# Kernel tuning notes

Measured on AMD Instinct MI355X. Metric: run time of the kernel, lower is better.

Reference implementation:

```python
import jax, jax.numpy as jnp
import numpy as np

N_NODES = 50000
N_EDGES = 640000
IN_CH = 128
OUT_CH = 128


def setup_inputs() -> dict:
    key = jax.random.key(0)
    k1, k2, k3, k4 = jax.random.split(key, 4)
    x = jax.random.normal(k1, (N_NODES, IN_CH), dtype=jnp.float32)
    edge_index = jax.random.randint(k2, (2, N_EDGES), 0, N_NODES, dtype=jnp.int32)
    # nn.Linear params: W [out, in], b [out]
    bound = 1.0 / np.sqrt(IN_CH)
    W = jax.random.uniform(k3, (OUT_CH, IN_CH), minval=-bound, maxval=bound, dtype=jnp.float32)
    b = jax.random.uniform(k4, (OUT_CH,), minval=-bound, maxval=bound, dtype=jnp.float32)
    return {"x": x, "edge_index": edge_index, "W": W, "b": b}


def reference(x, edge_index, W, b):
    row, col = edge_index[0], edge_index[1]
    num_nodes = x.shape[0]
    # degree of each destination node (clamped to >= 1)
    deg = jax.ops.segment_sum(jnp.ones(row.shape[0], dtype=x.dtype), row,
                              num_segments=num_nodes)
    deg = jnp.maximum(deg, 1.0)
    # gather neighbor features and scatter-add into destinations
    agg = jax.ops.segment_sum(x[col], row, num_segments=num_nodes)
    agg = agg / deg[:, None]
    # residual + linear
    return (x + agg) @ W.T + b
```

## Files before the change

### kernel.cpp

```cpp
#include <hip/hip_runtime.h>

#define N_NODES 50000
#define N_EDGES 640000
#define CH 128
#define NBINS 1563
#define NTILES 1563
#define BINB 256
#define EPB 2500
#define CAPR 48

typedef __bf16 bf16_t;
typedef bf16_t bf16x8 __attribute__((ext_vector_type(8)));
typedef float f32x4 __attribute__((ext_vector_type(4)));

__device__ __forceinline__ ushort f2bf(float f) {
  union { float f; unsigned u; } v; v.f = f;
  unsigned r = v.u + 0x7FFFu + ((v.u >> 16) & 1u);
  return (ushort)(r >> 16);
}
__device__ __forceinline__ float bflo(unsigned u) {
  union { unsigned u; float f; } v; v.u = u << 16; return v.f;
}
__device__ __forceinline__ float bfhi(unsigned u) {
  union { unsigned u; float f; } v; v.u = u & 0xFFFF0000u; return v.f;
}
__device__ __forceinline__ unsigned pack2(float lo, float hi) {
  return (unsigned)f2bf(lo) | ((unsigned)f2bf(hi) << 16);
}
__device__ __forceinline__ void addrow(float* acc, uint4 v) {
  acc[0] += bflo(v.x); acc[1] += bfhi(v.x);
  acc[2] += bflo(v.y); acc[3] += bfhi(v.y);
  acc[4] += bflo(v.z); acc[5] += bfhi(v.z);
  acc[6] += bflo(v.w); acc[7] += bfhi(v.w);
}


__global__ __launch_bounds__(256) void bink(const int* __restrict__ row,
                                            const int* __restrict__ col,
                                            unsigned* __restrict__ binRec,
                                            ushort* __restrict__ obot) {
  __shared__ int cnt[NBINS];
  __shared__ int parts[256];
  __shared__ __align__(16) unsigned recbuf[EPB];
  int bid = blockIdx.x;
  int tid = threadIdx.x;
  for (int i = tid; i < NBINS; i += 256) cnt[i] = 0;
  __syncthreads();
  int base = bid * EPB;
  int4 r4s[3], c4s[3];
  bool val[3];
#pragma unroll
  for (int b = 0; b < 3; ++b) {
    int idx4 = b * 1024 + tid * 4;
    val[b] = idx4 < EPB;
    if (val[b]) {
      r4s[b] = *(const int4*)(row + base + idx4);
      c4s[b] = *(const int4*)(col + base + idx4);
    }
  }
  unsigned pkv[12];
  unsigned colp[6];
#pragma unroll
  for (int b = 0; b < 3; ++b) {
    if (val[b]) {
      int rr[4] = {r4s[b].x, r4s[b].y, r4s[b].z, r4s[b].w};
      int cc[4] = {c4s[b].x, c4s[b].y, c4s[b].z, c4s[b].w};
#pragma unroll
      for (int j = 0; j < 4; ++j) {
        int bi = rr[j] >> 5;
        int rk = atomicAdd(&cnt[bi], 1);
        pkv[b * 4 + j] = ((unsigned)bi << 13) |
                         ((unsigned)(rr[j] & 31) << 8) | (unsigned)rk;
      }
      colp[b * 2]     = ((unsigned)cc[0] & 0xFFFFu) | ((unsigned)cc[1] << 16);
      colp[b * 2 + 1] = ((unsigned)cc[2] & 0xFFFFu) | ((unsigned)cc[3] << 16);
    } else {
#pragma unroll
      for (int j = 0; j < 4; ++j) pkv[b * 4 + j] = 0xFFFFFFFFu;
      colp[b * 2] = 0; colp[b * 2 + 1] = 0;
    }
  }
  __syncthreads();
  int c7[7];
  int s = 0;
#pragma unroll
  for (int k = 0; k < 7; ++k) {
    int i = tid * 7 + k;
    int c = (i < NBINS) ? cnt[i] : 0;
    c7[k] = c; s += c;
  }
  parts[tid] = s;
  __syncthreads();
  for (int off = 1; off < 256; off <<= 1) {
    int v = (tid >= off) ? parts[tid - off] : 0;
    __syncthreads();
    parts[tid] += v;
    __syncthreads();
  }
  int run = (tid > 0) ? parts[tid - 1] : 0;
#pragma unroll
  for (int k = 0; k < 7; ++k) {
    int i = tid * 7 + k;
    if (i < NBINS) {
      obot[i * BINB + bid] = (ushort)run;
      cnt[i] = run;
      run += c7[k];
    }
  }
  if (tid == 0) obot[NBINS * BINB + bid] = (ushort)EPB;
  __syncthreads();
#pragma unroll
  for (int k = 0; k < 12; ++k) {
    unsigned p = pkv[k];
    if (p != 0xFFFFFFFFu) {
      int bi = (int)(p >> 13);
      int lr5 = (int)((p >> 8) & 31u);
      int rk = (int)(p & 255u);
      unsigned cw = (colp[k >> 1] >> ((k & 1) * 16)) & 0xFFFFu;
      recbuf[cnt[bi] + rk] = ((unsigned)lr5 << 16) | cw;
    }
  }
  __syncthreads();
  uint4* gb4 = (uint4*)(binRec + base);
  const uint4* rb4 = (const uint4*)recbuf;
  for (int j = tid; j < EPB / 4; j += 256) gb4[j] = rb4[j];
}

__global__ __launch_bounds__(256) void conv(const float4* __restrict__ x4,
                                            uint4* __restrict__ xb4,
                                            const float4* __restrict__ W4,
                                            uint4* __restrict__ Wb4) {
  int bid = blockIdx.x;
  int tid = threadIdx.x;
  if (bid < 3125) {
    int i = bid * 256 + tid;
    float4 a = x4[i * 2], b = x4[i * 2 + 1];
    uint4 o;
    o.x = pack2(a.x, a.y); o.y = pack2(a.z, a.w);
    o.z = pack2(b.x, b.y); o.w = pack2(b.z, b.w);
    xb4[i] = o;
  } else {
    for (int i = tid; i < 2048; i += 256) {
      float4 c = W4[i * 2], d = W4[i * 2 + 1];
      uint4 w;
      w.x = pack2(c.x, c.y); w.y = pack2(c.z, c.w);
      w.z = pack2(d.x, d.y); w.w = pack2(d.z, d.w);
      Wb4[i] = w;
    }
  }
}

__global__ __launch_bounds__(512) void fused(const uint4* __restrict__ xb4,
                                             const unsigned* __restrict__ binRec,
                                             const ushort* __restrict__ obot,
                                             const uint4* __restrict__ Wb4,
                                             const float4* __restrict__ bias4,
                                             float4* __restrict__ out4) {
  __shared__ ushort hT[32 * CH];
  __shared__ __align__(16) ushort colL[32 * CAPR];
  __shared__ int rowcnt[32];
  int tid = threadIdx.x;
  int g = blockIdx.x;
  int m0 = g * 32;

  if (tid < 32) rowcnt[tid] = 0;
  __syncthreads();
  {
    int i = tid >> 1, sub = tid & 1;
    int o0 = obot[g * BINB + i];
    int o1 = obot[(g + 1) * BINB + i];
    const unsigned* rbase = binRec + i * EPB;
    for (int p = o0 + sub; p < o1; p += 2) {
      unsigned rec = rbase[p];
      int lr = (int)(rec >> 16);
      int pp = atomicAdd(&rowcnt[lr], 1);
      if (pp < CAPR) colL[lr * CAPR + pp] = (ushort)(rec & 0xFFFFu);
    }
  }
  __syncthreads();

  int wv = tid >> 6;
  int lane = tid & 63;
  int q = lane & 15;
  int grp = lane >> 4;
  int r = wv * 4 + grp;
  int node = m0 + r;
  int deg = rowcnt[r];
  int degc = deg < CAPR ? deg : CAPR;
  const ushort* arow = colL + r * CAPR;
  int nc = node < N_NODES ? node : 0;
  uint4 xi = xb4[nc * 16 + q];
  float acc[8] = {0.f, 0.f, 0.f, 0.f, 0.f, 0.f, 0.f, 0.f};
  int e = 0;
  for (; e + 7 < degc; e += 8) {
    uint4 ids = *(const uint4*)(arow + e);
    int n0 = ids.x & 0xFFFF, n1 = ids.x >> 16;
    int n2 = ids.y & 0xFFFF, n3 = ids.y >> 16;
    int n4 = ids.z & 0xFFFF, n5 = ids.z >> 16;
    int n6 = ids.w & 0xFFFF, n7 = ids.w >> 16;
    uint4 v0 = xb4[n0 * 16 + q];
    uint4 v1 = xb4[n1 * 16 + q];
    uint4 v2 = xb4[n2 * 16 + q];
    uint4 v3 = xb4[n3 * 16 + q];
    uint4 v4 = xb4[n4 * 16 + q];
    uint4 v5 = xb4[n5 * 16 + q];
    uint4 v6 = xb4[n6 * 16 + q];
    uint4 v7 = xb4[n7 * 16 + q];
    addrow(acc, v0); addrow(acc, v1); addrow(acc, v2); addrow(acc, v3);
    addrow(acc, v4); addrow(acc, v5); addrow(acc, v6); addrow(acc, v7);
  }
  if (e + 3 < degc) {
    uint2 ids = *(const uint2*)(arow + e);
    int n0 = ids.x & 0xFFFF, n1 = ids.x >> 16;
    int n2 = ids.y & 0xFFFF, n3 = ids.y >> 16;
    uint4 v0 = xb4[n0 * 16 + q];
    uint4 v1 = xb4[n1 * 16 + q];
    uint4 v2 = xb4[n2 * 16 + q];
    uint4 v3 = xb4[n3 * 16 + q];
    addrow(acc, v0); addrow(acc, v1); addrow(acc, v2); addrow(acc, v3);
    e += 4;
  }
  for (; e < degc; ++e) {
    uint4 v = xb4[(int)arow[e] * 16 + q];
    addrow(acc, v);
  }
  uint4 o = make_uint4(0, 0, 0, 0);
  if (node < N_NODES) {
    float s = 1.0f / fmaxf((float)deg, 1.0f);
    o.x = pack2(bflo(xi.x) + acc[0] * s, bfhi(xi.x) + acc[1] * s);
    o.y = pack2(bflo(xi.y) + acc[2] * s, bfhi(xi.y) + acc[3] * s);
    o.z = pack2(bflo(xi.z) + acc[4] * s, bfhi(xi.z) + acc[5] * s);
    o.w = pack2(bflo(xi.w) + acc[6] * s, bfhi(xi.w) + acc[7] * s);
  }
  *(uint4*)&hT[r * CH + ((q ^ (r & 15)) << 3)] = o;
  __syncthreads();

  int qq = grp;
  int mt = wv & 1;
  int nbase = (wv >> 1) * 2;
  const ushort* hbase = &hT[(mt * 16 + q) * CH];
  bf16x8 hb0 = *(const bf16x8*)(hbase + (((qq + 0) ^ q) << 3));
  bf16x8 hb1 = *(const bf16x8*)(hbase + (((qq + 4) ^ q) << 3));
  bf16x8 hb2 = *(const bf16x8*)(hbase + (((qq + 8) ^ q) << 3));
  bf16x8 hb3 = *(const bf16x8*)(hbase + (((qq + 12) ^ q) << 3));
  int m = m0 + mt * 16 + q;
#pragma unroll
  for (int i = 0; i < 2; ++i) {
    int nt = nbase + i;
    const uint4* wr = Wb4 + (nt * 16 + q) * 16 + qq;
    bf16x8 w0 = __builtin_bit_cast(bf16x8, wr[0]);
    bf16x8 w1 = __builtin_bit_cast(bf16x8, wr[4]);
    bf16x8 w2 = __builtin_bit_cast(bf16x8, wr[8]);
    bf16x8 w3 = __builtin_bit_cast(bf16x8, wr[12]);
    f32x4 acc2 = {0.f, 0.f, 0.f, 0.f};
    acc2 = __builtin_amdgcn_mfma_f32_16x16x32_bf16(w0, hb0, acc2, 0, 0, 0);
    acc2 = __builtin_amdgcn_mfma_f32_16x16x32_bf16(w1, hb1, acc2, 0, 0, 0);
    acc2 = __builtin_amdgcn_mfma_f32_16x16x32_bf16(w2, hb2, acc2, 0, 0, 0);
    acc2 = __builtin_amdgcn_mfma_f32_16x16x32_bf16(w3, hb3, acc2, 0, 0, 0);
    if (m < N_NODES) {
      float4 bv = bias4[nt * 4 + qq];
      f32x4 ov;
      ov.x = acc2[0] + bv.x;
      ov.y = acc2[1] + bv.y;
      ov.z = acc2[2] + bv.z;
      ov.w = acc2[3] + bv.w;
      __builtin_nontemporal_store(ov, (f32x4*)(out4 + (size_t)m * 32 + nt * 4 + qq));
    }
  }
}

extern "C" void kernel_launch(void* const* d_in, const int* in_sizes, int n_in,
                              void* d_out, int out_size, void* d_ws, size_t ws_size,
                              hipStream_t stream) {
  const float* x  = (const float*)d_in[0];
  const int*   ei = (const int*)d_in[1];
  const float* W  = (const float*)d_in[2];
  const float* bb = (const float*)d_in[3];

  char* ws = (char*)d_ws;
  unsigned* binRec = (unsigned*)ws;
  ushort*   obot   = (ushort*)(ws + 2560000);
  uint4*    Wb4    = (uint4*)(ws + 3360768);
  uint4*    xb4    = (uint4*)(ws + 3393536);

  bink<<<BINB, 256, 0, stream>>>(ei, ei + N_EDGES, binRec, obot);
  conv<<<3126, 256, 0, stream>>>((const float4*)x, xb4, (const float4*)W, Wb4);
  fused<<<NTILES, 512, 0, stream>>>(xb4, binRec, obot, Wb4,
                                    (const float4*)bb, (float4*)d_out);
}
```

Before: 133.1 us.

## Merge binning and bf16 conversion kernels, pad neighbor lists with zero row

The edge-binning kernel and the x/W bf16 conversion kernel become one launch, with branches on block index, so the two independent prep stages overlap and one launch is saved. Loads of x now use nontemporal hints. In the fused kernel each row's neighbor list is padded up to a multiple of 8 with a sentinel index that points at an extra zeroed row of xb4. This removes the 4-wide and scalar tail loops at the cost of extra gathers from that zero row. The zero row is written past the end of xb4, so the workspace must have room for it.

```diff
diff --git a/kernel.cpp b/kernel.cpp
--- a/kernel.cpp
+++ b/kernel.cpp
@@ -8,6 +8,7 @@
 #define BINB 256
 #define EPB 2500
 #define CAPR 48
+#define ZID N_NODES
 
 typedef __bf16 bf16_t;
 typedef bf16_t bf16x8 __attribute__((ext_vector_type(8)));
@@ -35,109 +36,107 @@
 }
 
 
-__global__ __launch_bounds__(256) void bink(const int* __restrict__ row,
+__global__ __launch_bounds__(256) void prep(const int* __restrict__ row,
                                             const int* __restrict__ col,
                                             unsigned* __restrict__ binRec,
-                                            ushort* __restrict__ obot) {
+                                            ushort* __restrict__ obot,
+                                            const f32x4* __restrict__ x4,
+                                            uint4* __restrict__ xb4,
+                                            const float4* __restrict__ W4,
+                                            uint4* __restrict__ Wb4) {
   __shared__ int cnt[NBINS];
   __shared__ int parts[256];
   __shared__ __align__(16) unsigned recbuf[EPB];
   int bid = blockIdx.x;
   int tid = threadIdx.x;
-  for (int i = tid; i < NBINS; i += 256) cnt[i] = 0;
-  __syncthreads();
-  int base = bid * EPB;
-  int4 r4s[3], c4s[3];
-  bool val[3];
-#pragma unroll
-  for (int b = 0; b < 3; ++b) {
-    int idx4 = b * 1024 + tid * 4;
-    val[b] = idx4 < EPB;
-    if (val[b]) {
-      r4s[b] = *(const int4*)(row + base + idx4);
-      c4s[b] = *(const int4*)(col + base + idx4);
-    }
-  }
-  unsigned pkv[12];
-  unsigned colp[6];
-#pragma unroll
-  for (int b = 0; b < 3; ++b) {
-    if (val[b]) {
-      int rr[4] = {r4s[b].x, r4s[b].y, r4s[b].z, r4s[b].w};
-      int cc[4] = {c4s[b].x, c4s[b].y, c4s[b].z, c4s[b].w};
-#pragma unroll
-      for (int j = 0; j < 4; ++j) {
-        int bi = rr[j] >> 5;
-        int rk = atomicAdd(&cnt[bi], 1);
-        pkv[b * 4 + j] = ((unsigned)bi << 13) |
-                         ((unsigned)(rr[j] & 31) << 8) | (unsigned)rk;
-      }
-      colp[b * 2]     = ((unsigned)cc[0] & 0xFFFFu) | ((unsigned)cc[1] << 16);
-      colp[b * 2 + 1] = ((unsigned)cc[2] & 0xFFFFu) | ((unsigned)cc[3] << 16);
-    } else {
-#pragma unroll
-      for (int j = 0; j < 4; ++j) pkv[b * 4 + j] = 0xFFFFFFFFu;
-      colp[b * 2] = 0; colp[b * 2 + 1] = 0;
-    }
-  }
-  __syncthreads();
-  int c7[7];
-  int s = 0;
-#pragma unroll
-  for (int k = 0; k < 7; ++k) {
-    int i = tid * 7 + k;
-    int c = (i < NBINS) ? cnt[i] : 0;
-    c7[k] = c; s += c;
-  }
-  parts[tid] = s;
-  __syncthreads();
-  for (int off = 1; off < 256; off <<= 1) {
-    int v = (tid >= off) ? parts[tid - off] : 0;
-    __syncthreads();
-    parts[tid] += v;
-    __syncthreads();
-  }
-  int run = (tid > 0) ? parts[tid - 1] : 0;
-#pragma unroll
-  for (int k = 0; k < 7; ++k) {
-    int i = tid * 7 + k;
-    if (i < NBINS) {
-      obot[i * BINB + bid] = (ushort)run;
-      cnt[i] = run;
-      run += c7[k];
-    }
-  }
-  if (tid == 0) obot[NBINS * BINB + bid] = (ushort)EPB;
-  __syncthreads();
-#pragma unroll
-  for (int k = 0; k < 12; ++k) {
-    unsigned p = pkv[k];
-    if (p != 0xFFFFFFFFu) {
-      int bi = (int)(p >> 13);
-      int lr5 = (int)((p >> 8) & 31u);
-      int rk = (int)(p & 255u);
-      unsigned cw = (colp[k >> 1] >> ((k & 1) * 16)) & 0xFFFFu;
-      recbuf[cnt[bi] + rk] = ((unsigned)lr5 << 16) | cw;
-    }
-  }
-  __syncthreads();
-  uint4* gb4 = (uint4*)(binRec + base);
-  const uint4* rb4 = (const uint4*)recbuf;
-  for (int j = tid; j < EPB / 4; j += 256) gb4[j] = rb4[j];
-}
-
-__global__ __launch_bounds__(256) void conv(const float4* __restrict__ x4,
-                                            uint4* __restrict__ xb4,
-                                            const float4* __restrict__ W4,
-                                            uint4* __restrict__ Wb4) {
-  int bid = blockIdx.x;
-  int tid = threadIdx.x;
-  if (bid < 3125) {
-    int i = bid * 256 + tid;
-    float4 a = x4[i * 2], b = x4[i * 2 + 1];
+  if (bid < BINB) {
+    for (int i = tid; i < NBINS; i += 256) cnt[i] = 0;
+    __syncthreads();
+    int base = bid * EPB;
+    int4 r4s[3], c4s[3];
+    bool val[3];
+#pragma unroll
+    for (int b = 0; b < 3; ++b) {
+      int idx4 = b * 1024 + tid * 4;
+      val[b] = idx4 < EPB;
+      if (val[b]) {
+        r4s[b] = *(const int4*)(row + base + idx4);
+        c4s[b] = *(const int4*)(col + base + idx4);
+      }
+    }
+    unsigned pkv[12];
+    unsigned colp[6];
+#pragma unroll
+    for (int b = 0; b < 3; ++b) {
+      if (val[b]) {
+        int rr[4] = {r4s[b].x, r4s[b].y, r4s[b].z, r4s[b].w};
+        int cc[4] = {c4s[b].x, c4s[b].y, c4s[b].z, c4s[b].w};
+#pragma unroll
+        for (int j = 0; j < 4; ++j) {
+          int bi = rr[j] >> 5;
+          int rk = atomicAdd(&cnt[bi], 1);
+          pkv[b * 4 + j] = ((unsigned)bi << 13) |
+                           ((unsigned)(rr[j] & 31) << 8) | (unsigned)rk;
+        }
+        colp[b * 2]     = ((unsigned)cc[0] & 0xFFFFu) | ((unsigned)cc[1] << 16);
+        colp[b * 2 + 1] = ((unsigned)cc[2] & 0xFFFFu) | ((unsigned)cc[3] << 16);
+      } else {
+#pragma unroll
+        for (int j = 0; j < 4; ++j) pkv[b * 4 + j] = 0xFFFFFFFFu;
+        colp[b * 2] = 0; colp[b * 2 + 1] = 0;
+      }
+    }
+    __syncthreads();
+    int c7[7];
+    int s = 0;
+#pragma unroll
+    for (int k = 0; k < 7; ++k) {
+      int i = tid * 7 + k;
+      int c = (i < NBINS) ? cnt[i] : 0;
+      c7[k] = c; s += c;
+    }
+    parts[tid] = s;
+    __syncthreads();
+    for (int off = 1; off < 256; off <<= 1) {
+      int v = (tid >= off) ? parts[tid - off] : 0;
+      __syncthreads();
+      parts[tid] += v;
+      __syncthreads();
+    }
+    int run = (tid > 0) ? parts[tid - 1] : 0;
+#pragma unroll
+    for (int k = 0; k < 7; ++k) {
+      int i = tid * 7 + k;
+      if (i < NBINS) {
+        obot[i * BINB + bid] = (ushort)run;
+        cnt[i] = run;
+        run += c7[k];
+      }
+    }
+    if (tid == 0) obot[NBINS * BINB + bid] = (ushort)EPB;
+    __syncthreads();
+#pragma unroll
+    for (int k = 0; k < 12; ++k) {
+      unsigned p = pkv[k];
+      if (p != 0xFFFFFFFFu) {
+        int bi = (int)(p >> 13);
+        int lr5 = (int)((p >> 8) & 31u);
+        int rk = (int)(p & 255u);
+        unsigned cw = (colp[k >> 1] >> ((k & 1) * 16)) & 0xFFFFu;
+        recbuf[cnt[bi] + rk] = ((unsigned)lr5 << 16) | cw;
+      }
+    }
+    __syncthreads();
+    uint4* gb4 = (uint4*)(binRec + base);
+    const uint4* rb4 = (const uint4*)recbuf;
+    for (int j = tid; j < EPB / 4; j += 256) gb4[j] = rb4[j];
+  } else if (bid < BINB + 3125) {
+    int i = (bid - BINB) * 256 + tid;
+    f32x4 a = __builtin_nontemporal_load(x4 + i * 2);
+    f32x4 b = __builtin_nontemporal_load(x4 + i * 2 + 1);
     uint4 o;
-    o.x = pack2(a.x, a.y); o.y = pack2(a.z, a.w);
-    o.z = pack2(b.x, b.y); o.w = pack2(b.z, b.w);
+    o.x = pack2(a[0], a[1]); o.y = pack2(a[2], a[3]);
+    o.z = pack2(b[0], b[1]); o.w = pack2(b[2], b[3]);
     xb4[i] = o;
   } else {
     for (int i = tid; i < 2048; i += 256) {
@@ -147,6 +146,7 @@
       w.z = pack2(d.x, d.y); w.w = pack2(d.z, d.w);
       Wb4[i] = w;
     }
+    if (tid < 16) xb4[ZID * 16 + tid] = make_uint4(0, 0, 0, 0);
   }
 }
 
@@ -178,6 +178,13 @@
     }
   }
   __syncthreads();
+  if (tid < 256) {
+    int r = tid >> 3, k = tid & 7;
+    int dc = rowcnt[r]; if (dc > CAPR) dc = CAPR;
+    int pc = (dc + 7) & ~7; if (pc > CAPR) pc = CAPR;
+    if (dc + k < pc) colL[r * CAPR + dc + k] = (ushort)ZID;
+  }
+  __syncthreads();
 
   int wv = tid >> 6;
   int lane = tid & 63;
@@ -187,12 +194,12 @@
   int node = m0 + r;
   int deg = rowcnt[r];
   int degc = deg < CAPR ? deg : CAPR;
+  int padc = (degc + 7) & ~7; if (padc > CAPR) padc = CAPR;
   const ushort* arow = colL + r * CAPR;
   int nc = node < N_NODES ? node : 0;
   uint4 xi = xb4[nc * 16 + q];
   float acc[8] = {0.f, 0.f, 0.f, 0.f, 0.f, 0.f, 0.f, 0.f};
-  int e = 0;
-  for (; e + 7 < degc; e += 8) {
+  for (int e = 0; e < padc; e += 8) {
     uint4 ids = *(const uint4*)(arow + e);
     int n0 = ids.x & 0xFFFF, n1 = ids.x >> 16;
     int n2 = ids.y & 0xFFFF, n3 = ids.y >> 16;
@@ -208,21 +215,6 @@
     uint4 v7 = xb4[n7 * 16 + q];
     addrow(acc, v0); addrow(acc, v1); addrow(acc, v2); addrow(acc, v3);
     addrow(acc, v4); addrow(acc, v5); addrow(acc, v6); addrow(acc, v7);
-  }
-  if (e + 3 < degc) {
-    uint2 ids = *(const uint2*)(arow + e);
-    int n0 = ids.x & 0xFFFF, n1 = ids.x >> 16;
-    int n2 = ids.y & 0xFFFF, n3 = ids.y >> 16;
-    uint4 v0 = xb4[n0 * 16 + q];
-    uint4 v1 = xb4[n1 * 16 + q];
-    uint4 v2 = xb4[n2 * 16 + q];
-    uint4 v3 = xb4[n3 * 16 + q];
-    addrow(acc, v0); addrow(acc, v1); addrow(acc, v2); addrow(acc, v3);
-    e += 4;
-  }
-  for (; e < degc; ++e) {
-    uint4 v = xb4[(int)arow[e] * 16 + q];
-    addrow(acc, v);
   }
   uint4 o = make_uint4(0, 0, 0, 0);
   if (node < N_NODES) {
@@ -283,8 +275,9 @@
   uint4*    Wb4    = (uint4*)(ws + 3360768);
   uint4*    xb4    = (uint4*)(ws + 3393536);
 
-  bink<<<BINB, 256, 0, stream>>>(ei, ei + N_EDGES, binRec, obot);
-  conv<<<3126, 256, 0, stream>>>((const float4*)x, xb4, (const float4*)W, Wb4);
+  prep<<<BINB + 3125 + 1, 256, 0, stream>>>(ei, ei + N_EDGES, binRec, obot,
+                                            (const f32x4*)x, xb4,
+                                            (const float4*)W, Wb4);
   fused<<<NTILES, 512, 0, stream>>>(xb4, binRec, obot, Wb4,
                                     (const float4*)bb, (float4*)d_out);
 }
```

Result: faster. 129.6 us (-2.6%).
